# Optimization experiments

Measured on AMD Instinct MI355X. Metric: run time of the kernel, lower is better.

## Reference

```python
import jax, jax.numpy as jnp
import numpy as np

N_LAYERS = 4
N_HEADS = 16

def layer_norm(x, s, b):
    m = jnp.mean(x, axis=-1, keepdims=True)
    v = jnp.mean((x - m) ** 2, axis=-1, keepdims=True)
    return (x - m) * jax.lax.rsqrt(v + 1e-5) * s + b

def patchify(x, p):
    # x: (N, c, H, W) -> (N, p*p, c*(H//p)*(W//p)); p patches per side
    N, c, H, W = x.shape
    ph, pw = H // p, W // p
    x = x.reshape(N, c, p, ph, p, pw).transpose(0, 2, 4, 1, 3, 5)
    return x.reshape(N, p * p, c * ph * pw)

def depatchify(x, p, c, ph, pw):
    # inverse of patchify: (N, p*p, c*ph*pw) -> (N, c, p*ph, p*pw)
    N = x.shape[0]
    x = x.reshape(N, p, p, c, ph, pw).transpose(0, 3, 1, 4, 2, 5)
    return x.reshape(N, c, p * ph, p * pw)

def _layer(x, allowed, wqkv, bqkv, wo, bo, s1, sb1, w1, fb1, w2, fb2, s2, sb2):
    B, S, D = x.shape
    hd = D // N_HEADS
    h = layer_norm(x, s1, sb1)
    q, k, v = jnp.split(h @ wqkv + bqkv, 3, axis=-1)
    q = q.reshape(B, S, N_HEADS, hd)
    k = k.reshape(B, S, N_HEADS, hd)
    v = v.reshape(B, S, N_HEADS, hd)
    scores = jnp.einsum('bqhd,bkhd->bhqk', q, k) * (hd ** -0.5)
    scores = jnp.where(allowed, scores, jnp.finfo(scores.dtype).min)
    a = jax.nn.softmax(scores, axis=-1)
    o = jnp.einsum('bhqk,bkhd->bqhd', a, v).reshape(B, S, D)
    x = x + o @ wo + bo
    h = layer_norm(x, s2, sb2)
    return x + jax.nn.gelu(h @ w1 + fb1) @ w2 + fb2

def _forward(f, g, pre_W, pre_b, post_W, post_b, patch_pos, func_pos,
             Wqkv, bqkv, Wo, bo, ln1_s, ln1_b, W1, b1, W2, b2, ln2_s, ln2_b):
    bs, pairs, c, H, W = f.shape
    p2, d = patch_pos.shape
    p = int(round(p2 ** 0.5))
    ph, pw = H // p, W // p
    # interleave condition/qoi: (bs, pairs, 2, c, H, W)
    x = jnp.concatenate((f[:, :, None], g[:, :, None]), axis=2)
    feat = patchify(x.reshape(bs * pairs * 2, c, H, W), p)      # (N, p2, c*ph*pw)
    feat = feat @ pre_W + pre_b + patch_pos                      # pre_proj + patch pos enc
    feat = feat.reshape(bs, pairs * 2, p2, d) + func_pos[:pairs * 2][None, :, None, :]
    S = pairs * 2 * p2
    feat = feat.reshape(bs, S, d)
    # alternating-block lower-triangular mask (uniform block size p2 since patch_num_in == patch_num_out)
    blocks = jnp.arange(S) // p2
    allowed = blocks[None, :] <= blocks[:, None]
    for i in range(N_LAYERS):
        feat = _layer(feat, allowed, Wqkv[i], bqkv[i], Wo[i], bo[i],
                      ln1_s[i], ln1_b[i], W1[i], b1[i], W2[i], b2[i], ln2_s[i], ln2_b[i])
    feat = feat.reshape(bs, pairs, 2, p2, d)[:, :, 0]            # keep condition-token outputs
    feat = feat @ post_W + post_b                                # post_proj
    feat = depatchify(feat.reshape(bs * pairs, p2, -1), p, c, ph, pw)
    feat = feat.reshape(bs, pairs, c, H, W)
    return feat[:, :-1], feat[:, -1:]                            # (ex_pred, qn_pred)

def setup_inputs():
    key = jax.random.key(0)
    ks = jax.random.split(key, 12)
    bs, pairs, c, H, W = 1, 5, 3, 128, 128
    p, d, dff, L = 16, 1024, 4096, N_LAYERS
    pin = c * (H // p) * (W // p)  # dim_channel * patch_resolution^2 = 192
    rn = lambda k, sh, sc: jax.random.normal(k, sh, jnp.float32) * sc
    return {
        'f': rn(ks[0], (bs, pairs, c, H, W), 1.0),
        'g': rn(ks[1], (bs, pairs, c, H, W), 1.0),
        'pre_W': rn(ks[2], (pin, d), 0.05), 'pre_b': jnp.zeros((d,), jnp.float32),
        'post_W': rn(ks[3], (d, pin), 0.03), 'post_b': jnp.zeros((pin,), jnp.float32),
        'patch_pos': rn(ks[4], (p * p, d), 0.02),
        'func_pos': rn(ks[5], (2 * pairs, d), 0.02),
        'Wqkv': rn(ks[6], (L, d, 3 * d), 0.03), 'bqkv': jnp.zeros((L, 3 * d), jnp.float32),
        'Wo': rn(ks[7], (L, d, d), 0.03), 'bo': jnp.zeros((L, d), jnp.float32),
        'ln1_s': jnp.ones((L, d), jnp.float32), 'ln1_b': jnp.zeros((L, d), jnp.float32),
        'W1': rn(ks[8], (L, d, dff), 0.03), 'b1': jnp.zeros((L, dff), jnp.float32),
        'W2': rn(ks[9], (L, dff, d), 0.02), 'b2': jnp.zeros((L, d), jnp.float32),
        'ln2_s': jnp.ones((L, d), jnp.float32), 'ln2_b': jnp.zeros((L, d), jnp.float32),
    }

def reference(f, g, pre_W, pre_b, post_W, post_b, patch_pos, func_pos,
              Wqkv, bqkv, Wo, bo, ln1_s, ln1_b, W1, b1, W2, b2, ln2_s, ln2_b):
    return _forward(f, g, pre_W, pre_b, post_W, post_b, patch_pos, func_pos,
                    Wqkv, bqkv, Wo, bo, ln1_s, ln1_b, W1, b1, W2, b2, ln2_s, ln2_b)
```

## Files before the change

kernel.cpp:

```cpp
#include <hip/hip_runtime.h>
#include <hip/hip_bf16.h>
#include <math.h>

#define DMODEL 1024
#define DFF    4096
#define NTOK   2560
#define PIN    192

typedef __attribute__((ext_vector_type(8))) __bf16 bf16x8;
typedef __attribute__((ext_vector_type(4))) __bf16 bf16x4;
typedef __attribute__((ext_vector_type(4))) float  f32x4;

#define MFMA16(a, b, c) __builtin_amdgcn_mfma_f32_16x16x32_bf16(a, b, c, 0, 0, 0)

__device__ __forceinline__ float gelu_f(float x) {
    const float x3 = x * x * x;
    return 0.5f * x * (1.0f + tanhf(0.7978845608028654f * (x + 0.044715f * x3)));
}

__device__ __forceinline__ void gload16(const void* g, void* l) {
    __builtin_amdgcn_global_load_lds((const __attribute__((address_space(1))) void*)g,
                                     (__attribute__((address_space(3))) void*)l, 16, 0, 0);
}

__device__ __forceinline__ void split_bf(float v, __bf16& hi, __bf16& lo) {
    hi = (__bf16)v;
    lo = (__bf16)(v - (float)hi);
}


__global__ __launch_bounds__(256) void patch_pre_kernel(
    const float* __restrict__ f, const float* __restrict__ g,
    const float* __restrict__ preW, const float* __restrict__ preb,
    const float* __restrict__ ppos, const float* __restrict__ fpos,
    float* __restrict__ out) {
    const int s0  = blockIdx.x * 4;
    const int tid = threadIdx.x;
    const int n    = s0 >> 8;
    const int pair = n >> 1, t = n & 1;
    const float* src = t ? g : f;

    __shared__ float patch[4][PIN];
    for (int l = tid; l < 4 * PIN; l += 256) {
        const int tok = l / PIN, kk = l - tok * PIN;
        const int pidx = (s0 & 255) + tok;
        const int cc = kk >> 6, a = (kk >> 3) & 7, b = kk & 7;
        const int i = pidx >> 4, j = pidx & 15;
        patch[tok][kk] = src[((size_t)(pair * 3 + cc) * 128 + (i * 8 + a)) * 128 + (j * 8 + b)];
    }
    __syncthreads();

    const int n0 = tid * 4;
    float acc[4][4] = {};
    for (int k = 0; k < PIN; ++k) {
        const float4 w = *(const float4*)(preW + (size_t)k * DMODEL + n0);
#pragma unroll
        for (int tok = 0; tok < 4; ++tok) {
            const float pv = patch[tok][k];
            acc[tok][0] += pv * w.x; acc[tok][1] += pv * w.y;
            acc[tok][2] += pv * w.z; acc[tok][3] += pv * w.w;
        }
    }
    const float4 pb = *(const float4*)(preb + n0);
    const float4 fp = *(const float4*)(fpos + (size_t)n * DMODEL + n0);
#pragma unroll
    for (int tok = 0; tok < 4; ++tok) {
        const int pidx = (s0 & 255) + tok;
        const float4 pp = *(const float4*)(ppos + (size_t)pidx * DMODEL + n0);
        float4 o;
        o.x = acc[tok][0] + pb.x + pp.x + fp.x;
        o.y = acc[tok][1] + pb.y + pp.y + fp.y;
        o.z = acc[tok][2] + pb.z + pp.z + fp.z;
        o.w = acc[tok][3] + pb.w + pp.w + fp.w;
        *(float4*)(out + (size_t)(s0 + tok) * DMODEL + n0) = o;
    }
}

__global__ __launch_bounds__(256) void wprep_kernel(
    const float* __restrict__ W, __bf16* __restrict__ WT, int K, int N) {
    const int n0 = blockIdx.x * 32, k0 = blockIdx.y * 32;
    const int tid = threadIdx.x;
    __shared__ float t[32][33];

    {
        const int kl = tid >> 3, nq = (tid & 7) * 4;
        const float4 v = *(const float4*)(W + (size_t)(k0 + kl) * N + n0 + nq);
        t[kl][nq] = v.x; t[kl][nq + 1] = v.y; t[kl][nq + 2] = v.z; t[kl][nq + 3] = v.w;
    }
    __syncthreads();

    const int nl = tid >> 3, kq = (tid & 7) * 4;
    const int n = n0 + nl;
    bf16x4 h4, l4;
#pragma unroll
    for (int i = 0; i < 4; ++i) {
        __bf16 hi, lo;
        split_bf(t[kq + i][nl], hi, lo);
        h4[i] = hi; l4[i] = lo;
    }
    const size_t base = (size_t)n * 2 * K + (size_t)(k0 >> 5) * 64 + (kq & 7);
    const int sl = kq >> 3, key = n & 7;
    *(bf16x4*)&WT[base + (size_t)((sl ^ key) << 3)]       = h4;
    *(bf16x4*)&WT[base + (size_t)(((sl | 4) ^ key) << 3)] = l4;
}

__global__ __launch_bounds__(256) void ln_split_kernel(
    const float* __restrict__ x, const float* __restrict__ gam,
    const float* __restrict__ bet, __bf16* __restrict__ o) {
    const int row = blockIdx.x, tid = threadIdx.x;
    const float* xr = x + (size_t)row * DMODEL;
    const float4 v = *(const float4*)(xr + tid * 4);

    __shared__ float red[4];
    __shared__ float stat[2];

    float s = v.x + v.y + v.z + v.w;
#pragma unroll
    for (int off = 32; off; off >>= 1) s += __shfl_down(s, off, 64);
    if ((tid & 63) == 0) red[tid >> 6] = s;
    __syncthreads();
    if (tid == 0) stat[0] = (red[0] + red[1] + red[2] + red[3]) * (1.0f / DMODEL);
    __syncthreads();
    const float m = stat[0];
    const float dx = v.x - m, dy = v.y - m, dz = v.z - m, dw = v.w - m;
    float ss = dx * dx + dy * dy + dz * dz + dw * dw;
#pragma unroll
    for (int off = 32; off; off >>= 1) ss += __shfl_down(ss, off, 64);
    if ((tid & 63) == 0) red[tid >> 6] = ss;
    __syncthreads();
    if (tid == 0) stat[1] = rsqrtf((red[0] + red[1] + red[2] + red[3]) * (1.0f / DMODEL) + 1e-5f);
    __syncthreads();
    const float rstd = stat[1];

    const float4 gv = *(const float4*)(gam + tid * 4);
    const float4 bv = *(const float4*)(bet + tid * 4);
    float ov[4];
    ov[0] = dx * rstd * gv.x + bv.x;
    ov[1] = dy * rstd * gv.y + bv.y;
    ov[2] = dz * rstd * gv.z + bv.z;
    ov[3] = dw * rstd * gv.w + bv.w;

    bf16x4 h4, l4;
#pragma unroll
    for (int i = 0; i < 4; ++i) {
        __bf16 hi, lo;
        split_bf(ov[i], hi, lo);
        h4[i] = hi; l4[i] = lo;
    }
    const int k0 = tid * 4;
    const size_t base = (size_t)row * 2048 + (size_t)(k0 >> 5) * 64 + (k0 & 7);
    const int sl = (k0 >> 3) & 3, key = row & 7;
    *(bf16x4*)&o[base + (size_t)((sl ^ key) << 3)]       = h4;
    *(bf16x4*)&o[base + (size_t)(((sl | 4) ^ key) << 3)] = l4;
}

template <int EPI>
__global__ __launch_bounds__(256) void gemm_mfma(
    const __bf16* __restrict__ A, const __bf16* __restrict__ B,
    const float* __restrict__ bias, float* __restrict__ resout,
    __bf16* __restrict__ bfout, int M, int N, int K) {
    __shared__ __bf16 sm[2][2][128 * 64];
    const int tid = threadIdx.x;
    const int w = tid >> 6, l = tid & 63;

    const int nwg = gridDim.x * gridDim.y;
    int bid = blockIdx.y * gridDim.x + blockIdx.x;
    bid = (bid & 7) * (nwg >> 3) + (bid >> 3);
    const int bn = bid % gridDim.x, bm = bid / gridDim.x;

    const int kz = blockIdx.z;
    const int nkTot = K >> 5;
    const int nk  = nkTot / gridDim.z;
    const int kb0 = kz * nk;

    const int mat = w >> 1, half = w & 1;
    const size_t rowBytes = (size_t)K * 4;
    const char* gsrc = (const char*)(mat ? B : A)
        + (size_t)((mat ? bn : bm) * 128 + half * 64 + (l >> 3)) * rowBytes
        + (size_t)(l & 7) * 16;

    auto STAGE = [&](int buf, int kbAbs) {
        const char* s = gsrc + (size_t)kbAbs * 128;
#pragma unroll
        for (int it = 0; it < 8; ++it)
            gload16(s + (size_t)(it * 8) * rowBytes,
                    (void*)&sm[buf][mat][(size_t)(half * 64 + it * 8) * 64]);
    };

    f32x4 acc[4][4];
#pragma unroll
    for (int i = 0; i < 4; ++i)
#pragma unroll
        for (int j = 0; j < 4; ++j) acc[i][j] = f32x4{0.f, 0.f, 0.f, 0.f};

    const int lr = l & 15, lk = l >> 4;
    const int wr = (w >> 1) * 64, wc = (w & 1) * 64;

    STAGE(0, kb0);
    __syncthreads();

    for (int kb = 0; kb < nk; ++kb) {
        const int buf = kb & 1;
        if (kb + 1 < nk) STAGE(buf ^ 1, kb0 + kb + 1);

        const __bf16* As = sm[buf][0];
        const __bf16* Bs = sm[buf][1];
        bf16x8 ah[4], al[4], bh[4], bl[4];
#pragma unroll
        for (int i = 0; i < 4; ++i) {
            const int row = wr + i * 16 + lr, kx = row & 7;
            ah[i] = *(const bf16x8*)&As[(size_t)row * 64 + ((lk ^ kx) << 3)];
            al[i] = *(const bf16x8*)&As[(size_t)row * 64 + (((lk | 4) ^ kx) << 3)];
            const int col = wc + i * 16 + lr, ky = col & 7;
            bh[i] = *(const bf16x8*)&Bs[(size_t)col * 64 + ((lk ^ ky) << 3)];
            bl[i] = *(const bf16x8*)&Bs[(size_t)col * 64 + (((lk | 4) ^ ky) << 3)];
        }
#pragma unroll
        for (int i = 0; i < 4; ++i)
#pragma unroll
            for (int j = 0; j < 4; ++j) {
                acc[i][j] = MFMA16(ah[i], bh[j], acc[i][j]);
                acc[i][j] = MFMA16(al[i], bh[j], acc[i][j]);
                acc[i][j] = MFMA16(ah[i], bl[j], acc[i][j]);
            }
        __syncthreads();
    }

#pragma unroll
    for (int j = 0; j < 4; ++j) {
        const int col = bn * 128 + wc + j * 16 + lr;
        const float bv = (EPI == 3) ? 0.f : bias[col];
#pragma unroll
        for (int i = 0; i < 4; ++i) {
#pragma unroll
            for (int r = 0; r < 4; ++r) {
                const int rr = bm * 128 + wr + i * 16 + lk * 4 + r;
                const float v = acc[i][j][r] + bv;
                if (EPI == 0) {
                    bfout[(size_t)rr * N + col] = (__bf16)v;
                } else if (EPI == 1) {
                    resout[(size_t)rr * N + col] += v;
                } else if (EPI == 3) {
                    resout[((size_t)kz * M + rr) * N + col] = acc[i][j][r];
                } else {
                    const float gv2 = gelu_f(v);
                    __bf16 hi, lo;
                    split_bf(gv2, hi, lo);
                    const size_t base = (size_t)rr * 2 * N + (size_t)(col >> 5) * 64 + (col & 7);
                    const int sl = (col >> 3) & 3, kx = rr & 7;
                    bfout[base + (size_t)((sl ^ kx) << 3)]       = hi;
                    bfout[base + (size_t)(((sl | 4) ^ kx) << 3)] = lo;
                }
            }
        }
    }
}

__global__ __launch_bounds__(256) void reduce_splitk(
    const float* __restrict__ part, const float* __restrict__ bias,
    float* __restrict__ x, int MN, int N) {
    const int i = (blockIdx.x * 256 + threadIdx.x) * 4;
    if (i >= MN) return;
    const float4 p0 = *(const float4*)(part + i);
    const float4 p1 = *(const float4*)(part + (size_t)MN + i);
    const float4 bv = *(const float4*)(bias + (i & (N - 1)));
    float4 xv = *(float4*)(x + i);
    xv.x += p0.x + p1.x + bv.x;
    xv.y += p0.y + p1.y + bv.y;
    xv.z += p0.z + p1.z + bv.z;
    xv.w += p0.w + p1.w + bv.w;
    *(float4*)(x + i) = xv;
}

__global__ __launch_bounds__(256) void attn_mfma(
    const __bf16* __restrict__ qkv, __bf16* __restrict__ o) {
    const int lin = blockIdx.y * gridDim.x + blockIdx.x;
    const int h  = ((lin & 7) << 1) | ((lin >> 3) & 1);
    const int qb = lin >> 4;
    const int tid = threadIdx.x;
    const int w = tid >> 6, l = tid & 63;
    const int lr = l & 15, lk = l >> 4;

    __shared__ __bf16 Ks[64 * 64];
    __shared__ __bf16 Vt[64 * 64];
    __shared__ __bf16 Ps[4][16 * 64];

    const int qrow = qb * 64 + w * 16 + lr;
    const __bf16* qsrc = qkv + (size_t)qrow * 3072 + h * 64 + lk * 8;
    const bf16x8 qf0 = *(const bf16x8*)qsrc;
    const bf16x8 qf1 = *(const bf16x8*)(qsrc + 32);

    f32x4 oacc[4];
#pragma unroll
    for (int i = 0; i < 4; ++i) oacc[i] = f32x4{0.f, 0.f, 0.f, 0.f};
    float mrow[4], lrow[4];
#pragma unroll
    for (int r = 0; r < 4; ++r) { mrow[r] = -3.0e38f; lrow[r] = 0.f; }

    const int skey = tid >> 2, dc = (tid & 3) * 16;
    const int nch = ((qb >> 2) + 1) * 4;

    for (int kc = 0; kc < nch; ++kc) {
        __syncthreads();
        {
            const __bf16* kp = qkv + (size_t)(kc * 64 + skey) * 3072 + 1024 + h * 64 + dc;
            const bf16x8 k0 = *(const bf16x8*)kp;
            const bf16x8 k1 = *(const bf16x8*)(kp + 8);
            const int sl0 = dc >> 3;
            *(bf16x8*)&Ks[skey * 64 + ((sl0 ^ (skey & 7)) << 3)]       = k0;
            *(bf16x8*)&Ks[skey * 64 + (((sl0 | 1) ^ (skey & 7)) << 3)] = k1;

            const __bf16* vp = kp + 1024;
            const bf16x8 v0 = *(const bf16x8*)vp;
            const bf16x8 v1 = *(const bf16x8*)(vp + 8);
#pragma unroll
            for (int e = 0; e < 8; ++e) {
                const int d0 = dc + e, d1 = dc + 8 + e;
                Vt[d0 * 64 + (((skey >> 3) ^ (d0 & 7)) << 3) + (skey & 7)] = v0[e];
                Vt[d1 * 64 + (((skey >> 3) ^ (d1 & 7)) << 3) + (skey & 7)] = v1[e];
            }
        }
        __syncthreads();

        f32x4 sv[4];
#pragma unroll
        for (int j = 0; j < 4; ++j) {
            sv[j] = f32x4{0.f, 0.f, 0.f, 0.f};
            const int kb = j * 16 + lr, sw = kb & 7;
            const bf16x8 kb0 = *(const bf16x8*)&Ks[kb * 64 + ((lk ^ sw) << 3)];
            const bf16x8 kb1 = *(const bf16x8*)&Ks[kb * 64 + (((lk | 4) ^ sw) << 3)];
            sv[j] = MFMA16(qf0, kb0, sv[j]);
            sv[j] = MFMA16(qf1, kb1, sv[j]);
        }

#pragma unroll
        for (int r = 0; r < 4; ++r) {
            float cm = fmaxf(fmaxf(sv[0][r], sv[1][r]), fmaxf(sv[2][r], sv[3][r])) * 0.125f;
#pragma unroll
            for (int msk = 1; msk < 16; msk <<= 1) cm = fmaxf(cm, __shfl_xor(cm, msk, 64));
            const float nm = fmaxf(mrow[r], cm);
            const float sc = __expf(mrow[r] - nm);
            float rs = 0.f;
#pragma unroll
            for (int j = 0; j < 4; ++j) {
                const float p = __expf(sv[j][r] * 0.125f - nm);
                sv[j][r] = p;
                rs += p;
            }
#pragma unroll
            for (int msk = 1; msk < 16; msk <<= 1) rs += __shfl_xor(rs, msk, 64);
            lrow[r] = lrow[r] * sc + rs;
            mrow[r] = nm;
#pragma unroll
            for (int db = 0; db < 4; ++db) oacc[db][r] *= sc;
        }

#pragma unroll
        for (int j = 0; j < 4; ++j)
#pragma unroll
            for (int r = 0; r < 4; ++r) {
                const int q = lk * 4 + r, key = j * 16 + lr;
                Ps[w][q * 64 + (((key >> 3) ^ (q & 7)) << 3) + (key & 7)] = (__bf16)sv[j][r];
            }
        asm volatile("" ::: "memory");

#pragma unroll
        for (int db = 0; db < 4; ++db) {
            const int d = db * 16 + lr, dw2 = d & 7;
#pragma unroll
            for (int kk = 0; kk < 2; ++kk) {
                const int sl = kk * 4 + lk;
                const bf16x8 pa = *(const bf16x8*)&Ps[w][lr * 64 + ((sl ^ (lr & 7)) << 3)];
                const bf16x8 vb = *(const bf16x8*)&Vt[d * 64 + ((sl ^ dw2) << 3)];
                oacc[db] = MFMA16(pa, vb, oacc[db]);
            }
        }
    }

    float inv[4];
#pragma unroll
    for (int r = 0; r < 4; ++r) inv[r] = 1.0f / lrow[r];

#pragma unroll
    for (int db = 0; db < 4; ++db)
#pragma unroll
        for (int r = 0; r < 4; ++r) {
            const float v = oacc[db][r] * inv[r];
            const int rr = qb * 64 + w * 16 + lk * 4 + r;
            const int col = h * 64 + db * 16 + lr;
            __bf16 hi, lo;
            split_bf(v, hi, lo);
            const size_t base = (size_t)rr * 2048 + (size_t)(col >> 5) * 64 + (col & 7);
            const int sl = (col >> 3) & 3, kx = rr & 7;
            o[base + (size_t)((sl ^ kx) << 3)]       = hi;
            o[base + (size_t)(((sl | 4) ^ kx) << 3)] = lo;
        }
}

template <int EPI>
__global__ __launch_bounds__(256) void gemm64k(
    const float* __restrict__ A, const float* __restrict__ B,
    const float* __restrict__ bias, const float* __restrict__ res,
    float* __restrict__ C, int M, int N, int K) {
    __shared__ float As[16][64];
    __shared__ float Bs[16][64];
    const int tid = threadIdx.x;
    const int bm = blockIdx.y, bn = blockIdx.x;
    const int tx = tid & 15, ty = tid >> 4;

    float acc[4][4] = {};

    const int am = tid & 63, ka = (tid >> 6) * 4;
    const int bnn = tid & 63, kb = (tid >> 6) * 4;
    const float* Ap = A + (size_t)(bm * 64 + am) * K + ka;
    const float* Bp = B + (size_t)kb * N + bn * 64 + bnn;

    for (int kt = 0; kt < K; kt += 16) {
        const float4 a0 = *(const float4*)Ap;
        const float b0 = Bp[0];
        const float b1 = Bp[(size_t)N];
        const float b2 = Bp[(size_t)2 * N];
        const float b3 = Bp[(size_t)3 * N];
        __syncthreads();
        As[ka + 0][am] = a0.x; As[ka + 1][am] = a0.y; As[ka + 2][am] = a0.z; As[ka + 3][am] = a0.w;
        Bs[kb + 0][bnn] = b0; Bs[kb + 1][bnn] = b1; Bs[kb + 2][bnn] = b2; Bs[kb + 3][bnn] = b3;
        __syncthreads();
#pragma unroll
        for (int kk = 0; kk < 16; ++kk) {
            float a[4], b[4];
            *(float4*)&a[0] = *(const float4*)&As[kk][ty * 4];
            *(float4*)&b[0] = *(const float4*)&Bs[kk][tx * 4];
#pragma unroll
            for (int i = 0; i < 4; ++i)
#pragma unroll
                for (int j = 0; j < 4; ++j)
                    acc[i][j] += a[i] * b[j];
        }
        Ap += 16;
        Bp += (size_t)16 * N;
    }

    const int col0 = bn * 64 + tx * 4;
    const float4 bv = *(const float4*)(bias + col0);
    const float* bvp = (const float*)&bv;
#pragma unroll
    for (int i = 0; i < 4; ++i) {
        const int row = bm * 64 + ty * 4 + i;
        float o0[4];
#pragma unroll
        for (int j = 0; j < 4; ++j) o0[j] = acc[i][j] + bvp[j];
        if (EPI == 1) {
            const float4 r0 = *(const float4*)(res + (size_t)row * N + col0);
            o0[0] += r0.x; o0[1] += r0.y; o0[2] += r0.z; o0[3] += r0.w;
        }
        *(float4*)(C + (size_t)row * N + col0) = make_float4(o0[0], o0[1], o0[2], o0[3]);
    }
}

__global__ __launch_bounds__(256) void gather_f_kernel(
    const float* __restrict__ x, float* __restrict__ ftok) {
    const int r = blockIdx.x;
    const int pair = r >> 8, pidx = r & 255;
    const int srow = pair * 512 + pidx;
    const int c = threadIdx.x * 4;
    *(float4*)(ftok + (size_t)r * DMODEL + c) = *(const float4*)(x + (size_t)srow * DMODEL + c);
}

__global__ __launch_bounds__(192) void depatch_kernel(
    const float* __restrict__ pbuf, float* __restrict__ out) {
    const int r = blockIdx.x;
    const int tid = threadIdx.x;
    const int pair = r >> 8, pidx = r & 255;
    const int i = pidx >> 4, j = pidx & 15;
    const int cc = tid >> 6, a = (tid >> 3) & 7, b = tid & 7;
    out[((size_t)(pair * 3 + cc) * 128 + (i * 8 + a)) * 128 + (j * 8 + b)] =
        pbuf[(size_t)r * PIN + tid];
}

extern "C" void kernel_launch(void* const* d_in, const int* in_sizes, int n_in,
                              void* d_out, int out_size, void* d_ws, size_t ws_size,
                              hipStream_t stream) {
    const float* f     = (const float*)d_in[0];
    const float* g     = (const float*)d_in[1];
    const float* preW  = (const float*)d_in[2];
    const float* preb  = (const float*)d_in[3];
    const float* postW = (const float*)d_in[4];
    const float* postb = (const float*)d_in[5];
    const float* ppos  = (const float*)d_in[6];
    const float* fpos  = (const float*)d_in[7];
    const float* Wqkv  = (const float*)d_in[8];
    const float* bqkv  = (const float*)d_in[9];
    const float* Wo    = (const float*)d_in[10];
    const float* bo    = (const float*)d_in[11];
    const float* ln1s  = (const float*)d_in[12];
    const float* ln1b  = (const float*)d_in[13];
    const float* W1    = (const float*)d_in[14];
    const float* b1w   = (const float*)d_in[15];
    const float* W2    = (const float*)d_in[16];
    const float* b2w   = (const float*)d_in[17];
    const float* ln2s  = (const float*)d_in[18];
    const float* ln2b  = (const float*)d_in[19];
    float* out = (float*)d_out;

    char* p = (char*)d_ws;
    float*  x      = (float*)p;   p += (size_t)NTOK * DMODEL * 4;
    __bf16* hbufs  = (__bf16*)p;  p += (size_t)NTOK * 2048 * 2;
    __bf16* obufs  = (__bf16*)p;  p += (size_t)NTOK * 2048 * 2;
    char*   unionA = p;           p += (size_t)NTOK * 8192 * 2;
    __bf16* wT     = (__bf16*)p;  p += (size_t)4096 * 2048 * 2;

    __bf16* qkvbf = (__bf16*)unionA;
    float*  partO = (float*)unionA;
    __bf16* acts  = (__bf16*)unionA;
    float*  partM = (float*)hbufs;
    float*  ftok  = (float*)unionA;
    float*  pbuf  = (float*)(unionA + (size_t)1280 * DMODEL * 4);

    patch_pre_kernel<<<NTOK / 4, 256, 0, stream>>>(f, g, preW, preb, ppos, fpos, x);

    for (int L = 0; L < 4; ++L) {
        ln_split_kernel<<<NTOK, 256, 0, stream>>>(x, ln1s + L * DMODEL, ln1b + L * DMODEL, hbufs);
        wprep_kernel<<<dim3(3072 / 32, 1024 / 32), 256, 0, stream>>>(
            Wqkv + (size_t)L * 1024 * 3072, wT, 1024, 3072);
        gemm_mfma<0><<<dim3(24, 20), 256, 0, stream>>>(
            hbufs, wT, bqkv + (size_t)L * 3072, nullptr, qkvbf, NTOK, 3072, 1024);
        attn_mfma<<<dim3(16, 40), 256, 0, stream>>>(qkvbf, obufs);
        wprep_kernel<<<dim3(1024 / 32, 1024 / 32), 256, 0, stream>>>(
            Wo + (size_t)L * 1024 * 1024, wT, 1024, 1024);
        gemm_mfma<3><<<dim3(8, 20, 2), 256, 0, stream>>>(
            obufs, wT, nullptr, partO, nullptr, NTOK, 1024, 1024);
        reduce_splitk<<<NTOK, 256, 0, stream>>>(partO, bo + (size_t)L * DMODEL, x,
                                                NTOK * DMODEL, DMODEL);
        ln_split_kernel<<<NTOK, 256, 0, stream>>>(x, ln2s + L * DMODEL, ln2b + L * DMODEL, hbufs);
        wprep_kernel<<<dim3(4096 / 32, 1024 / 32), 256, 0, stream>>>(
            W1 + (size_t)L * 1024 * 4096, wT, 1024, 4096);
        gemm_mfma<2><<<dim3(32, 20), 256, 0, stream>>>(
            hbufs, wT, b1w + (size_t)L * DFF, nullptr, acts, NTOK, 4096, 1024);
        wprep_kernel<<<dim3(1024 / 32, 4096 / 32), 256, 0, stream>>>(
            W2 + (size_t)L * 4096 * 1024, wT, 4096, 1024);
        gemm_mfma<3><<<dim3(8, 20, 2), 256, 0, stream>>>(
            acts, wT, nullptr, partM, nullptr, NTOK, 1024, 4096);
        reduce_splitk<<<NTOK, 256, 0, stream>>>(partM, b2w + (size_t)L * DMODEL, x,
                                                NTOK * DMODEL, DMODEL);
    }

    gather_f_kernel<<<1280, 256, 0, stream>>>(x, ftok);
    gemm64k<0><<<dim3(PIN / 64, 1280 / 64), 256, 0, stream>>>(
        ftok, postW, postb, nullptr, pbuf, 1280, PIN, 1024);
    depatch_kernel<<<1280, 192, 0, stream>>>(pbuf, out);
}
```

Measured before the change: 1.740 ms.

## Emit transposed V from QKV GEMM and widen attention key chunks to 128

The QKV GEMM epilogue now writes Q/K into a 2048-wide buffer and V directly in a pre-transposed, token-permuted per-chunk layout. This removes the scalar LDS transpose of V inside attention. The attention kernel processes 128-key chunks with vectorized K/V loads, pre-scales Q by the softmax scale, packs P into a bf16x8 store, adds s_setprio around the MFMA blocks, and launches query blocks in reverse order so the heaviest causal blocks start first. The cost is scattered 2-byte global stores in the GEMM epilogue for the V part, plus larger LDS use and register pressure in attention.

```diff
diff --git a/kernel.cpp b/kernel.cpp
--- a/kernel.cpp
+++ b/kernel.cpp
@@ -158,7 +158,7 @@
 __global__ __launch_bounds__(256) void gemm_mfma(
     const __bf16* __restrict__ A, const __bf16* __restrict__ B,
     const float* __restrict__ bias, float* __restrict__ resout,
-    __bf16* __restrict__ bfout, int M, int N, int K) {
+    __bf16* __restrict__ bfout, __bf16* __restrict__ vtout, int M, int N, int K) {
     __shared__ __bf16 sm[2][2][128 * 64];
     const int tid = threadIdx.x;
     const int w = tid >> 6, l = tid & 63;
@@ -237,7 +237,14 @@
                 const int rr = bm * 128 + wr + i * 16 + lk * 4 + r;
                 const float v = acc[i][j][r] + bv;
                 if (EPI == 0) {
-                    bfout[(size_t)rr * N + col] = (__bf16)v;
+                    if (col < 2048) {
+                        bfout[(size_t)rr * 2048 + col] = (__bf16)v;
+                    } else {
+                        const int hv = col - 2048, hh = hv >> 6, dd = hv & 63;
+                        const int tok = rr & 127, chn = rr >> 7;
+                        const int tokp = (tok & 15) * 8 + (tok >> 4);
+                        vtout[(((size_t)chn * 16 + hh) * 64 + dd) * 128 + tokp] = (__bf16)v;
+                    }
                 } else if (EPI == 1) {
                     resout[(size_t)rr * N + col] += v;
                 } else if (EPI == 3) {
@@ -273,78 +280,97 @@
 }
 
 __global__ __launch_bounds__(256) void attn_mfma(
-    const __bf16* __restrict__ qkv, __bf16* __restrict__ o) {
+    const __bf16* __restrict__ qk, const __bf16* __restrict__ vt,
+    __bf16* __restrict__ o) {
     const int lin = blockIdx.y * gridDim.x + blockIdx.x;
     const int h  = ((lin & 7) << 1) | ((lin >> 3) & 1);
-    const int qb = lin >> 4;
+    const int qb = 39 - (lin >> 4);
     const int tid = threadIdx.x;
     const int w = tid >> 6, l = tid & 63;
     const int lr = l & 15, lk = l >> 4;
 
-    __shared__ __bf16 Ks[64 * 64];
-    __shared__ __bf16 Vt[64 * 64];
-    __shared__ __bf16 Ps[4][16 * 64];
+    __shared__ __bf16 Ks[128 * 64];
+    __shared__ __bf16 Vs[64 * 128];
+    __shared__ __bf16 Ps[4][16 * 128];
+
+    const f32x4 Z4 = {0.f, 0.f, 0.f, 0.f};
 
     const int qrow = qb * 64 + w * 16 + lr;
-    const __bf16* qsrc = qkv + (size_t)qrow * 3072 + h * 64 + lk * 8;
-    const bf16x8 qf0 = *(const bf16x8*)qsrc;
-    const bf16x8 qf1 = *(const bf16x8*)(qsrc + 32);
+    const __bf16* qsrc = qk + (size_t)qrow * 2048 + h * 64 + lk * 8;
+    bf16x8 qf0 = *(const bf16x8*)qsrc;
+    bf16x8 qf1 = *(const bf16x8*)(qsrc + 32);
+#pragma unroll
+    for (int e = 0; e < 8; ++e) {
+        qf0[e] = (__bf16)((float)qf0[e] * 0.125f);
+        qf1[e] = (__bf16)((float)qf1[e] * 0.125f);
+    }
 
     f32x4 oacc[4];
 #pragma unroll
-    for (int i = 0; i < 4; ++i) oacc[i] = f32x4{0.f, 0.f, 0.f, 0.f};
+    for (int i = 0; i < 4; ++i) oacc[i] = Z4;
     float mrow[4], lrow[4];
 #pragma unroll
     for (int r = 0; r < 4; ++r) { mrow[r] = -3.0e38f; lrow[r] = 0.f; }
 
-    const int skey = tid >> 2, dc = (tid & 3) * 16;
-    const int nch = ((qb >> 2) + 1) * 4;
+    const int kKey = w * 32 + (l >> 1), kHalf = l & 1;
+    const int vD   = w * 16 + (l >> 2), vC4  = l & 3;
+
+    const int nch = ((qb >> 2) + 1) * 2;
 
     for (int kc = 0; kc < nch; ++kc) {
         __syncthreads();
         {
-            const __bf16* kp = qkv + (size_t)(kc * 64 + skey) * 3072 + 1024 + h * 64 + dc;
-            const bf16x8 k0 = *(const bf16x8*)kp;
-            const bf16x8 k1 = *(const bf16x8*)(kp + 8);
-            const int sl0 = dc >> 3;
-            *(bf16x8*)&Ks[skey * 64 + ((sl0 ^ (skey & 7)) << 3)]       = k0;
-            *(bf16x8*)&Ks[skey * 64 + (((sl0 | 1) ^ (skey & 7)) << 3)] = k1;
-
-            const __bf16* vp = kp + 1024;
-            const bf16x8 v0 = *(const bf16x8*)vp;
-            const bf16x8 v1 = *(const bf16x8*)(vp + 8);
-#pragma unroll
-            for (int e = 0; e < 8; ++e) {
-                const int d0 = dc + e, d1 = dc + 8 + e;
-                Vt[d0 * 64 + (((skey >> 3) ^ (d0 & 7)) << 3) + (skey & 7)] = v0[e];
-                Vt[d1 * 64 + (((skey >> 3) ^ (d1 & 7)) << 3) + (skey & 7)] = v1[e];
-            }
+            const __bf16* kp = qk + (size_t)(kc * 128 + kKey) * 2048 + 1024 + h * 64 + kHalf * 32;
+            bf16x8 kv0 = ((const bf16x8*)kp)[0];
+            bf16x8 kv1 = ((const bf16x8*)kp)[1];
+            bf16x8 kv2 = ((const bf16x8*)kp)[2];
+            bf16x8 kv3 = ((const bf16x8*)kp)[3];
+            const int ksw = kKey & 7;
+            *(bf16x8*)&Ks[kKey * 64 + (((kHalf * 4 + 0) ^ ksw) << 3)] = kv0;
+            *(bf16x8*)&Ks[kKey * 64 + (((kHalf * 4 + 1) ^ ksw) << 3)] = kv1;
+            *(bf16x8*)&Ks[kKey * 64 + (((kHalf * 4 + 2) ^ ksw) << 3)] = kv2;
+            *(bf16x8*)&Ks[kKey * 64 + (((kHalf * 4 + 3) ^ ksw) << 3)] = kv3;
+
+            const __bf16* vp = vt + (((size_t)(kc * 16 + h) * 64 + vD) * 128) + vC4 * 32;
+            bf16x8 vv0 = ((const bf16x8*)vp)[0];
+            bf16x8 vv1 = ((const bf16x8*)vp)[1];
+            bf16x8 vv2 = ((const bf16x8*)vp)[2];
+            bf16x8 vv3 = ((const bf16x8*)vp)[3];
+            const int vsw = vD & 15;
+            *(bf16x8*)&Vs[vD * 128 + (((vC4 * 4 + 0) ^ vsw) << 3)] = vv0;
+            *(bf16x8*)&Vs[vD * 128 + (((vC4 * 4 + 1) ^ vsw) << 3)] = vv1;
+            *(bf16x8*)&Vs[vD * 128 + (((vC4 * 4 + 2) ^ vsw) << 3)] = vv2;
+            *(bf16x8*)&Vs[vD * 128 + (((vC4 * 4 + 3) ^ vsw) << 3)] = vv3;
         }
         __syncthreads();
 
-        f32x4 sv[4];
-#pragma unroll
-        for (int j = 0; j < 4; ++j) {
-            sv[j] = f32x4{0.f, 0.f, 0.f, 0.f};
+        f32x4 sv[8];
+        __builtin_amdgcn_s_setprio(1);
+#pragma unroll
+        for (int j = 0; j < 8; ++j) {
             const int kb = j * 16 + lr, sw = kb & 7;
             const bf16x8 kb0 = *(const bf16x8*)&Ks[kb * 64 + ((lk ^ sw) << 3)];
             const bf16x8 kb1 = *(const bf16x8*)&Ks[kb * 64 + (((lk | 4) ^ sw) << 3)];
-            sv[j] = MFMA16(qf0, kb0, sv[j]);
+            sv[j] = MFMA16(qf0, kb0, Z4);
             sv[j] = MFMA16(qf1, kb1, sv[j]);
         }
+        __builtin_amdgcn_s_setprio(0);
 
 #pragma unroll
         for (int r = 0; r < 4; ++r) {
-            float cm = fmaxf(fmaxf(sv[0][r], sv[1][r]), fmaxf(sv[2][r], sv[3][r])) * 0.125f;
+            float cm = sv[0][r];
+#pragma unroll
+            for (int j = 1; j < 8; ++j) cm = fmaxf(cm, sv[j][r]);
 #pragma unroll
             for (int msk = 1; msk < 16; msk <<= 1) cm = fmaxf(cm, __shfl_xor(cm, msk, 64));
             const float nm = fmaxf(mrow[r], cm);
             const float sc = __expf(mrow[r] - nm);
             float rs = 0.f;
-#pragma unroll
-            for (int j = 0; j < 4; ++j) {
-                const float p = __expf(sv[j][r] * 0.125f - nm);
-                sv[j][r] = p;
+            bf16x8 pv;
+#pragma unroll
+            for (int j = 0; j < 8; ++j) {
+                const float p = __expf(sv[j][r] - nm);
+                pv[j] = (__bf16)p;
                 rs += p;
             }
 #pragma unroll
@@ -353,28 +379,26 @@
             mrow[r] = nm;
 #pragma unroll
             for (int db = 0; db < 4; ++db) oacc[db][r] *= sc;
-        }
-
-#pragma unroll
-        for (int j = 0; j < 4; ++j)
-#pragma unroll
-            for (int r = 0; r < 4; ++r) {
-                const int q = lk * 4 + r, key = j * 16 + lr;
-                Ps[w][q * 64 + (((key >> 3) ^ (q & 7)) << 3) + (key & 7)] = (__bf16)sv[j][r];
+            const int q = lk * 4 + r;
+            *(bf16x8*)&Ps[w][q * 128 + ((lr ^ q) << 3)] = pv;
+        }
+        asm volatile("" ::: "memory");
+
+        bf16x8 pa[4];
+#pragma unroll
+        for (int ksl = 0; ksl < 4; ++ksl)
+            pa[ksl] = *(const bf16x8*)&Ps[w][lr * 128 + (((ksl * 4 + lk) ^ lr) << 3)];
+        __builtin_amdgcn_s_setprio(1);
+#pragma unroll
+        for (int db = 0; db < 4; ++db) {
+            const int d = db * 16 + lr, dsw = d & 15;
+#pragma unroll
+            for (int ksl = 0; ksl < 4; ++ksl) {
+                const bf16x8 vb = *(const bf16x8*)&Vs[d * 128 + (((ksl * 4 + lk) ^ dsw) << 3)];
+                oacc[db] = MFMA16(pa[ksl], vb, oacc[db]);
             }
-        asm volatile("" ::: "memory");
-
-#pragma unroll
-        for (int db = 0; db < 4; ++db) {
-            const int d = db * 16 + lr, dw2 = d & 7;
-#pragma unroll
-            for (int kk = 0; kk < 2; ++kk) {
-                const int sl = kk * 4 + lk;
-                const bf16x8 pa = *(const bf16x8*)&Ps[w][lr * 64 + ((sl ^ (lr & 7)) << 3)];
-                const bf16x8 vb = *(const bf16x8*)&Vt[d * 64 + ((sl ^ dw2) << 3)];
-                oacc[db] = MFMA16(pa, vb, oacc[db]);
-            }
-        }
+        }
+        __builtin_amdgcn_s_setprio(0);
     }
 
     float inv[4];
@@ -509,7 +533,8 @@
     char*   unionA = p;           p += (size_t)NTOK * 8192 * 2;
     __bf16* wT     = (__bf16*)p;  p += (size_t)4096 * 2048 * 2;
 
-    __bf16* qkvbf = (__bf16*)unionA;
+    __bf16* qk_bf = (__bf16*)unionA;
+    __bf16* vt_bf = (__bf16*)(unionA + (size_t)NTOK * 2048 * 2);
     float*  partO = (float*)unionA;
     __bf16* acts  = (__bf16*)unionA;
     float*  partM = (float*)hbufs;
@@ -523,23 +548,23 @@
         wprep_kernel<<<dim3(3072 / 32, 1024 / 32), 256, 0, stream>>>(
             Wqkv + (size_t)L * 1024 * 3072, wT, 1024, 3072);
         gemm_mfma<0><<<dim3(24, 20), 256, 0, stream>>>(
-            hbufs, wT, bqkv + (size_t)L * 3072, nullptr, qkvbf, NTOK, 3072, 1024);
-        attn_mfma<<<dim3(16, 40), 256, 0, stream>>>(qkvbf, obufs);
+            hbufs, wT, bqkv + (size_t)L * 3072, nullptr, qk_bf, vt_bf, NTOK, 3072, 1024);
+        attn_mfma<<<dim3(16, 40), 256, 0, stream>>>(qk_bf, vt_bf, obufs);
         wprep_kernel<<<dim3(1024 / 32, 1024 / 32), 256, 0, stream>>>(
             Wo + (size_t)L * 1024 * 1024, wT, 1024, 1024);
         gemm_mfma<3><<<dim3(8, 20, 2), 256, 0, stream>>>(
-            obufs, wT, nullptr, partO, nullptr, NTOK, 1024, 1024);
+            obufs, wT, nullptr, partO, nullptr, nullptr, NTOK, 1024, 1024);
         reduce_splitk<<<NTOK, 256, 0, stream>>>(partO, bo + (size_t)L * DMODEL, x,
                                                 NTOK * DMODEL, DMODEL);
         ln_split_kernel<<<NTOK, 256, 0, stream>>>(x, ln2s + L * DMODEL, ln2b + L * DMODEL, hbufs);
         wprep_kernel<<<dim3(4096 / 32, 1024 / 32), 256, 0, stream>>>(
             W1 + (size_t)L * 1024 * 4096, wT, 1024, 4096);
         gemm_mfma<2><<<dim3(32, 20), 256, 0, stream>>>(
-            hbufs, wT, b1w + (size_t)L * DFF, nullptr, acts, NTOK, 4096, 1024);
+            hbufs, wT, b1w + (size_t)L * DFF, nullptr, acts, nullptr, NTOK, 4096, 1024);
         wprep_kernel<<<dim3(1024 / 32, 4096 / 32), 256, 0, stream>>>(
             W2 + (size_t)L * 4096 * 1024, wT, 4096, 1024);
         gemm_mfma<3><<<dim3(8, 20, 2), 256, 0, stream>>>(
-            acts, wT, nullptr, partM, nullptr, NTOK, 1024, 4096);
+            acts, wT, nullptr, partM, nullptr, nullptr, NTOK, 1024, 4096);
         reduce_splitk<<<NTOK, 256, 0, stream>>>(partM, b2w + (size_t)L * DMODEL, x,
                                                 NTOK * DMODEL, DMODEL);
     }
```

Result: faster. 1.661 ms (-4.5%).
